# Performance work log

Measured on AMD Instinct MI355X. Metric: run time of the kernel, lower is better.

## Reference

```python
import jax, jax.numpy as jnp
import numpy as np

N_NODES = 50000
N_EDGES = 800000
IN_DIM, HID_DIM, OUT_DIM = 64, 128, 64


def gcn_conv(x, src, dst, W, b, n_nodes):
    # PyG GCNConv default: add self-loops, symmetric normalization D^-1/2 A D^-1/2
    h = x @ W  # [N, F_out]
    ones = jnp.ones(src.shape[0], dtype=x.dtype)
    deg = jax.ops.segment_sum(ones, dst, num_segments=n_nodes)  # in-degree incl. self-loops
    dinv = jnp.where(deg > 0, jax.lax.rsqrt(deg), 0.0).astype(x.dtype)
    norm = dinv[src] * dinv[dst]  # [E]
    msg = h[src] * norm[:, None]  # gather + scale, [E, F_out]
    out = jax.ops.segment_sum(msg, dst, num_segments=n_nodes)  # scatter-add
    return out + b


def setup_inputs() -> dict:
    key = jax.random.key(0)
    k1, k2, k3, k4 = jax.random.split(key, 4)
    z = jax.random.normal(k1, (N_NODES, IN_DIM), dtype=jnp.float32)
    edge_index = jax.random.randint(k2, (2, N_EDGES), 0, N_NODES, dtype=jnp.int64)
    # Glorot-style init for weights, zero bias (PyG defaults)
    W1 = jax.random.normal(k3, (IN_DIM, HID_DIM), dtype=jnp.float32) / np.sqrt(IN_DIM)
    b1 = jnp.zeros((HID_DIM,), dtype=jnp.float32)
    W2 = jax.random.normal(k4, (HID_DIM, OUT_DIM), dtype=jnp.float32) / np.sqrt(HID_DIM)
    b2 = jnp.zeros((OUT_DIM,), dtype=jnp.float32)
    return {"z": z, "edge_index": edge_index, "W1": W1, "b1": b1, "W2": W2, "b2": b2}


def reference(z, edge_index, W1, b1, W2, b2):
    n = z.shape[0]
    loops = jnp.arange(n, dtype=edge_index.dtype)
    src = jnp.concatenate([edge_index[0], loops])
    dst = jnp.concatenate([edge_index[1], loops])
    h = jax.nn.relu(gcn_conv(z, src, dst, W1, b1, n))
    x_hat = gcn_conv(h, src, dst, W2, b2, n)
    return x_hat
```

## Files before the change

### kernel.cpp

```cpp
#include <hip/hip_runtime.h>
#include <hip/hip_bf16.h>

#define N_NODES 50000
#define N_EDGES 800000
#define IN_DIM 64
#define HID_DIM 128
#define OUT_DIM 64
#define NGRP 8
#define NSLC 4
#define NPB 32
#define ECAP 2048
#define NE8 (NGRP * N_NODES)
#define NC8C ((NE8 + 255) / 256)
#define NCMC ((N_NODES + 255) / 256)

__device__ int g_in_f32;
__device__ int g_is64;
__device__ int g_csr[N_EDGES];
__device__ int g_mcsr[N_EDGES];
__device__ int g_deg8[NE8];
__device__ int g_rowptr8[NE8 + 1];
__device__ int g_cursor8[NE8];
__device__ int g_mrp[N_NODES + 1];
__device__ int g_bsum[NC8C];
__device__ int g_bsum2[NCMC];
__device__ float g_dinv[N_NODES];
__device__ __align__(16) float g_W1f[IN_DIM * HID_DIM];
__device__ __align__(16) float g_W2f[HID_DIM * OUT_DIM];
__device__ __align__(16) float g_b1f[HID_DIM];
__device__ __align__(16) float g_b2f[OUT_DIM];
__device__ __align__(16) float g_hs1[(size_t)N_NODES * IN_DIM];
__device__ __align__(16) float g_agg1[(size_t)N_NODES * IN_DIM];

__device__ __forceinline__ float loadx(const void* p, int i, int f32) {
    if (f32) return ((const float*)p)[i];
    unsigned int u = ((unsigned int)((const unsigned short*)p)[i]) << 16;
    return __uint_as_float(u);
}

__global__ __launch_bounds__(256) void zerodet_kernel(const unsigned short* __restrict__ zw,
                                                      const unsigned int* __restrict__ ew,
                                                      int NE, int E) {
    int idx = blockIdx.x * 256 + threadIdx.x;
    if (idx < NE) g_deg8[idx] = 0;
    if (blockIdx.x == 0) {
        __shared__ int flags[2];
        int t = threadIdx.x;
        if (t < 2) flags[t] = 0;
        __syncthreads();
        int hit = 0;
        for (int k = 0; k < 64; k++) {
            int i = 2 * ((t * 64 + k) * 97);
            if (((zw[i] >> 7) & 0xFF) == 0xFF) hit = 1;
        }
        if (hit) atomicOr(&flags[0], 1);
        int nz = 0;
        int step = E / 4096;
        for (int k = 0; k < 4; k++) {
            int i = 1 + 2 * ((t * 4 + k) * step);
            if (ew[i] != 0) nz = 1;
        }
        if (nz) atomicOr(&flags[1], 1);
        __syncthreads();
        if (t == 0) { g_in_f32 = flags[0]; g_is64 = (flags[1] == 0) ? 1 : 0; }
    }
}

__global__ __launch_bounds__(256) void degprep_kernel(const void* __restrict__ ei,
                                                      const void* __restrict__ W1, const void* __restrict__ b1,
                                                      const void* __restrict__ W2, const void* __restrict__ b2,
                                                      int N, int E) {
    int e = blockIdx.x * 256 + threadIdx.x;
    int f32 = g_in_f32;
    if (e < IN_DIM * HID_DIM) g_W1f[e] = loadx(W1, e, f32);
    if (e < HID_DIM * OUT_DIM) g_W2f[e] = loadx(W2, e, f32);
    if (e < HID_DIM) g_b1f[e] = loadx(b1, e, f32);
    if (e < OUT_DIM) g_b2f[e] = loadx(b2, e, f32);
    if (e < E) {
        int d = g_is64 ? (int)((const long long*)ei)[E + e] : ((const int*)ei)[E + e];
        int g = blockIdx.x & (NGRP - 1);
        atomicAdd(&g_deg8[g * N + d], 1);
    }
}

__global__ __launch_bounds__(256) void scans_kernel(int N, int NE) {
    __shared__ int sc[256];
    int t = threadIdx.x;
    int NC8 = (NE + 255) >> 8, NCM = (N + 255) >> 8;
    for (int vb = blockIdx.x; vb < NC8; vb += gridDim.x) {
        int idx = (vb << 8) + t;
        int d = (idx < NE) ? g_deg8[idx] : 0;
        sc[t] = d;
        __syncthreads();
        for (int off = 1; off < 256; off <<= 1) {
            int v = (t >= off) ? sc[t - off] : 0;
            __syncthreads();
            sc[t] += v;
            __syncthreads();
        }
        if (idx < NE) g_rowptr8[idx] = sc[t] - d;
        if (t == 255) g_bsum[vb] = sc[255];
        __syncthreads();
    }
    for (int vb = blockIdx.x; vb < NCM; vb += gridDim.x) {
        int idx = (vb << 8) + t;
        int d = 0;
        if (idx < N) {
#pragma unroll
            for (int g = 0; g < NGRP; g++) d += g_deg8[g * N + idx];
            g_dinv[idx] = rsqrtf((float)d + 1.0f);
        }
        sc[t] = d;
        __syncthreads();
        for (int off = 1; off < 256; off <<= 1) {
            int v = (t >= off) ? sc[t - off] : 0;
            __syncthreads();
            sc[t] += v;
            __syncthreads();
        }
        if (idx < N) g_mrp[idx] = sc[t] - d;
        if (t == 255) g_bsum2[vb] = sc[255];
        __syncthreads();
    }
}

__global__ __launch_bounds__(256) void addoffs_kernel(int N, int NE, int E) {
    __shared__ int sc[256];
    int t = threadIdx.x;
    int vb = blockIdx.x;
    int NCM = (N + 255) >> 8;
    int ps = 0;
    for (int i = t; i < vb; i += 256) ps += g_bsum[i];
    sc[t] = ps;
    __syncthreads();
    for (int off = 128; off > 0; off >>= 1) {
        if (t < off) sc[t] += sc[t + off];
        __syncthreads();
    }
    int prefix = sc[0];
    __syncthreads();
    int idx = vb * 256 + t;
    if (idx < NE) {
        int base = g_rowptr8[idx] + prefix;
        g_rowptr8[idx] = base;
        g_cursor8[idx] = base;
    }
    if (vb < NCM) {
        int ps2 = 0;
        for (int i = t; i < vb; i += 256) ps2 += g_bsum2[i];
        sc[t] = ps2;
        __syncthreads();
        for (int off = 128; off > 0; off >>= 1) {
            if (t < off) sc[t] += sc[t + off];
            __syncthreads();
        }
        int prefix2 = sc[0];
        if (idx < N) g_mrp[idx] += prefix2;
    }
    if (vb == 0 && t == 0) { g_rowptr8[NE] = E; g_mrp[N] = E; }
}

__global__ __launch_bounds__(256) void scatter_kernel(const void* __restrict__ ei, int N, int E) {
    int e = blockIdx.x * 256 + threadIdx.x;
    if (e < E) {
        int s, d;
        if (g_is64) { const long long* p = (const long long*)ei; s = (int)p[e]; d = (int)p[E + e]; }
        else        { const int* p = (const int*)ei; s = p[e]; d = p[E + e]; }
        int g = blockIdx.x & (NGRP - 1);
        int pos = atomicAdd(&g_cursor8[g * N + d], 1);
        g_csr[pos] = s;
    }
}

__global__ __launch_bounds__(256) void mergezp_kernel(const void* __restrict__ z, int N) {
    int gid = blockIdx.x * 256 + threadIdx.x;
    int wid = gid >> 6;
    int lane = threadIdx.x & 63;
    if (wid < N) {
        int mybeg = 0, mycnt = 0;
        if (lane < NGRP) {
            mybeg = g_rowptr8[lane * N + wid];
            mycnt = g_rowptr8[lane * N + wid + 1] - mybeg;
        }
        int incl = mycnt;
#pragma unroll
        for (int off = 1; off < NGRP; off <<= 1) {
            int v = __shfl_up(incl, off, 64);
            if (lane >= off) incl += v;
        }
        int myoff = incl - mycnt;
        int go[NGRP], gb[NGRP];
#pragma unroll
        for (int k = 0; k < NGRP; k++) {
            go[k] = __shfl(myoff, k, 64);
            gb[k] = __shfl(mybeg, k, 64);
        }
        int total = __shfl(incl, NGRP - 1, 64);
        int base = g_mrp[wid];
        for (int i = lane; i < total; i += 64) {
            int g = 0;
#pragma unroll
            for (int k = 1; k < NGRP; k++) g += (i >= go[k]);
            g_mcsr[base + i] = g_csr[gb[g] + i - go[g]];
        }
    }
    if (gid < N * IN_DIM) {
        int node = gid >> 6, c = gid & 63;
        int s = c >> 4, off = c & 15;
        g_agg1[(size_t)s * (N * 16) + node * 16 + off] = loadx(z, gid, g_in_f32) * g_dinv[node];
    }
}

template <int LAYER2>
__global__ __launch_bounds__(256) void aggslc_kernel(void* __restrict__ outp, int N) {
    __shared__ int rp[NPB + 1];
    __shared__ int eidx[ECAP];
    int s = blockIdx.x & (NSLC - 1);
    int n0 = (blockIdx.x >> 2) * NPB;
    int t = threadIdx.x;
    if (t <= NPB) {
        int idx = n0 + t;
        rp[t] = g_mrp[idx <= N ? idx : N];
    }
    __syncthreads();
    int base = rp[0];
    int range = rp[NPB] - base;
    bool staged = (range <= ECAP);
    if (staged) {
        for (int i = t; i < range; i += 256) eidx[i] = g_mcsr[base + i];
    }
    __syncthreads();
    const float* tab = (LAYER2 ? g_hs1 : g_agg1) + (size_t)s * ((size_t)N * 16);
    int lane = t & 63;
    int w8 = (t >> 6) * 8;
    int col = lane & 15, eslot = lane >> 4;
    float res[8];
#pragma unroll
    for (int k = 0; k < 8; k++) {
        int jb = rp[w8 + k] - base + eslot;
        int je = rp[w8 + k + 1] - base;
        float a0 = 0.f, a1 = 0.f, a2 = 0.f, a3 = 0.f;
        int j = jb;
        if (staged) {
            for (; j + 12 < je; j += 16) {
                int i0 = eidx[j], i1 = eidx[j + 4], i2 = eidx[j + 8], i3 = eidx[j + 12];
                a0 += tab[i0 * 16 + col];
                a1 += tab[i1 * 16 + col];
                a2 += tab[i2 * 16 + col];
                a3 += tab[i3 * 16 + col];
            }
            for (; j < je; j += 4) a0 += tab[eidx[j] * 16 + col];
        } else {
            for (; j < je; j += 4) a0 += tab[g_mcsr[base + j] * 16 + col];
        }
        float a = (a0 + a1) + (a2 + a3);
        a += __shfl_xor(a, 16, 64);
        a += __shfl_xor(a, 32, 64);
        res[k] = a;
    }
    if (lane < 16) {
#pragma unroll
        for (int k = 0; k < 8; k++) {
            int nk = n0 + w8 + k;
            if (nk < N) {
                float v = (res[k] + tab[(size_t)nk * 16 + col]) * g_dinv[nk];
                if (LAYER2) {
                    v += g_b2f[s * 16 + col];
                    int oc = nk * 64 + s * 16 + col;
                    if (g_in_f32) ((float*)outp)[oc] = v;
                    else ((__hip_bfloat16*)outp)[oc] = __float2bfloat16(v);
                } else {
                    g_hs1[(size_t)s * ((size_t)N * 16) + nk * 16 + col] = v;
                }
            }
        }
    }
}

__global__ __launch_bounds__(256) void gemm_fused_kernel(int N) {
    __shared__ __align__(16) float B[64 * 132];
    int t = threadIdx.x;
    int row0 = blockIdx.x * 64;
#pragma unroll
    for (int s = 0; s < 4; s++) {
        int i = t + s * 256;
        int r = i >> 4, k4 = i & 15;
        int row = row0 + r;
        int g = k4 >> 2, off = (k4 & 3) * 4;
        float4 v = make_float4(0.f, 0.f, 0.f, 0.f);
        if (row < N) v = *(const float4*)&g_hs1[(size_t)g * (N * 16) + row * 16 + off];
        *(float4*)&B[r * 132 + k4 * 4] = v;
    }
    __syncthreads();
    int cg1 = t & 31, rg1 = t >> 5;
    int c1 = cg1 * 4, r1 = rg1 * 8;
    float acc1[8][4] = {};
#pragma unroll 4
    for (int k = 0; k < IN_DIM; k++) {
        float b[4];
        *(float4*)b = *(const float4*)&g_W1f[k * HID_DIM + c1];
        float a[8];
#pragma unroll
        for (int i = 0; i < 8; i++) a[i] = B[(r1 + i) * 132 + k];
#pragma unroll
        for (int i = 0; i < 8; i++)
#pragma unroll
            for (int j = 0; j < 4; j++) acc1[i][j] = fmaf(a[i], b[j], acc1[i][j]);
    }
    __syncthreads();
    {
        float4 bias = *(const float4*)&g_b1f[c1];
#pragma unroll
        for (int i = 0; i < 8; i++) {
            float4 v;
            v.x = fmaxf(acc1[i][0] + bias.x, 0.f);
            v.y = fmaxf(acc1[i][1] + bias.y, 0.f);
            v.z = fmaxf(acc1[i][2] + bias.z, 0.f);
            v.w = fmaxf(acc1[i][3] + bias.w, 0.f);
            *(float4*)&B[(r1 + i) * 132 + c1] = v;
        }
    }
    __syncthreads();
    {
        int cg = t & 15, rg = t >> 4;
        int c0 = cg * 4, r0 = rg * 4;
        float acc[4][4] = {};
#pragma unroll 2
        for (int k4 = 0; k4 < 32; k4++) {
            float av[4][4];
#pragma unroll
            for (int i = 0; i < 4; i++)
                *(float4*)av[i] = *(const float4*)&B[(r0 + i) * 132 + k4 * 4];
#pragma unroll
            for (int jj = 0; jj < 4; jj++) {
                float b[4];
                *(float4*)b = *(const float4*)&g_W2f[(k4 * 4 + jj) * OUT_DIM + c0];
#pragma unroll
                for (int i = 0; i < 4; i++)
#pragma unroll
                    for (int j = 0; j < 4; j++) acc[i][j] = fmaf(av[i][jj], b[j], acc[i][j]);
            }
        }
        int g = cg >> 2, off = (cg & 3) * 4;
#pragma unroll
        for (int i = 0; i < 4; i++) {
            int row = row0 + r0 + i;
            if (row < N) {
                float dn = g_dinv[row];
                float4 v;
                v.x = acc[i][0] * dn;
                v.y = acc[i][1] * dn;
                v.z = acc[i][2] * dn;
                v.w = acc[i][3] * dn;
                *(float4*)&g_hs1[(size_t)g * (N * 16) + row * 16 + off] = v;
            }
        }
    }
}

extern "C" void kernel_launch(void* const* d_in, const int* in_sizes, int n_in,
                              void* d_out, int out_size, void* d_ws, size_t ws_size,
                              hipStream_t stream) {
    const void* z  = d_in[0];
    const void* ei = d_in[1];
    const void* W1 = d_in[2];
    const void* b1 = d_in[3];
    const void* W2 = d_in[4];
    const void* b2 = d_in[5];

    const int N = in_sizes[0] / IN_DIM;
    const int E = in_sizes[1] / 2;
    const int NE = NGRP * N;
    const int NC8 = (NE + 255) / 256;
    const int aggblocks = NSLC * ((N + NPB - 1) / NPB);

    zerodet_kernel<<<NC8, 256, 0, stream>>>((const unsigned short*)z, (const unsigned int*)ei, NE, E);
    degprep_kernel<<<(E + 255) / 256, 256, 0, stream>>>(ei, W1, b1, W2, b2, N, E);
    scans_kernel<<<NC8, 256, 0, stream>>>(N, NE);
    addoffs_kernel<<<NC8, 256, 0, stream>>>(N, NE, E);
    scatter_kernel<<<(E + 255) / 256, 256, 0, stream>>>(ei, N, E);
    mergezp_kernel<<<(N * 64 + 255) / 256, 256, 0, stream>>>(z, N);

    aggslc_kernel<0><<<aggblocks, 256, 0, stream>>>(d_out, N);
    gemm_fused_kernel<<<(N + 63) / 64, 256, 0, stream>>>(N);
    aggslc_kernel<1><<<aggblocks, 256, 0, stream>>>(d_out, N);
}
```

Measured before the change: 301.3 us.

## Remap aggregation threads to float4 per node and double nodes per block

The gather-aggregate kernel now gives each node to four lanes, each loading a float4 of its 16-column slice. Before, a wavefront walked 8 nodes in turn with scalar loads and reduced across lanes with shuffles. The goal is wider memory transactions, no shuffle reductions, and more nodes in flight per block, with NPB doubled from 32 to 64. In exchange, per-lane load imbalance follows node degree, and the larger node block makes it more likely that a block's edge count exceeds the shared staging capacity, which sends it to the unstaged fallback path.

```diff
diff --git a/kernel.cpp b/kernel.cpp
--- a/kernel.cpp
+++ b/kernel.cpp
@@ -8,7 +8,7 @@
 #define OUT_DIM 64
 #define NGRP 8
 #define NSLC 4
-#define NPB 32
+#define NPB 64
 #define ECAP 2048
 #define NE8 (NGRP * N_NODES)
 #define NC8C ((NE8 + 255) / 256)
@@ -232,48 +232,55 @@
     __syncthreads();
     const float* tab = (LAYER2 ? g_hs1 : g_agg1) + (size_t)s * ((size_t)N * 16);
     int lane = t & 63;
-    int w8 = (t >> 6) * 8;
-    int col = lane & 15, eslot = lane >> 4;
-    float res[8];
-#pragma unroll
-    for (int k = 0; k < 8; k++) {
-        int jb = rp[w8 + k] - base + eslot;
-        int je = rp[w8 + k + 1] - base;
-        float a0 = 0.f, a1 = 0.f, a2 = 0.f, a3 = 0.f;
+    int nsub = (t >> 6) * 16 + (lane >> 2);
+    int col4 = lane & 3;
+    int nk = n0 + nsub;
+    if (nk >= N) return;
+    float4 a0 = make_float4(0.f, 0.f, 0.f, 0.f);
+    float4 a1 = make_float4(0.f, 0.f, 0.f, 0.f);
+    int jb = rp[nsub] - base;
+    int je = rp[nsub + 1] - base;
+    if (staged) {
         int j = jb;
-        if (staged) {
-            for (; j + 12 < je; j += 16) {
-                int i0 = eidx[j], i1 = eidx[j + 4], i2 = eidx[j + 8], i3 = eidx[j + 12];
-                a0 += tab[i0 * 16 + col];
-                a1 += tab[i1 * 16 + col];
-                a2 += tab[i2 * 16 + col];
-                a3 += tab[i3 * 16 + col];
-            }
-            for (; j < je; j += 4) a0 += tab[eidx[j] * 16 + col];
+        for (; j + 1 < je; j += 2) {
+            int i0 = eidx[j], i1 = eidx[j + 1];
+            float4 v0 = *(const float4*)&tab[(size_t)i0 * 16 + col4 * 4];
+            float4 v1 = *(const float4*)&tab[(size_t)i1 * 16 + col4 * 4];
+            a0.x += v0.x; a0.y += v0.y; a0.z += v0.z; a0.w += v0.w;
+            a1.x += v1.x; a1.y += v1.y; a1.z += v1.z; a1.w += v1.w;
+        }
+        if (j < je) {
+            float4 v0 = *(const float4*)&tab[(size_t)eidx[j] * 16 + col4 * 4];
+            a0.x += v0.x; a0.y += v0.y; a0.z += v0.z; a0.w += v0.w;
+        }
+    } else {
+        for (int j = jb; j < je; j++) {
+            float4 v0 = *(const float4*)&tab[(size_t)g_mcsr[base + j] * 16 + col4 * 4];
+            a0.x += v0.x; a0.y += v0.y; a0.z += v0.z; a0.w += v0.w;
+        }
+    }
+    float4 self = *(const float4*)&tab[(size_t)nk * 16 + col4 * 4];
+    float dn = g_dinv[nk];
+    float4 v;
+    v.x = (a0.x + a1.x + self.x) * dn;
+    v.y = (a0.y + a1.y + self.y) * dn;
+    v.z = (a0.z + a1.z + self.z) * dn;
+    v.w = (a0.w + a1.w + self.w) * dn;
+    if (LAYER2) {
+        float4 bias = *(const float4*)&g_b2f[s * 16 + col4 * 4];
+        v.x += bias.x; v.y += bias.y; v.z += bias.z; v.w += bias.w;
+        int oc = nk * 64 + s * 16 + col4 * 4;
+        if (g_in_f32) {
+            *(float4*)&((float*)outp)[oc] = v;
         } else {
-            for (; j < je; j += 4) a0 += tab[g_mcsr[base + j] * 16 + col];
-        }
-        float a = (a0 + a1) + (a2 + a3);
-        a += __shfl_xor(a, 16, 64);
-        a += __shfl_xor(a, 32, 64);
-        res[k] = a;
-    }
-    if (lane < 16) {
-#pragma unroll
-        for (int k = 0; k < 8; k++) {
-            int nk = n0 + w8 + k;
-            if (nk < N) {
-                float v = (res[k] + tab[(size_t)nk * 16 + col]) * g_dinv[nk];
-                if (LAYER2) {
-                    v += g_b2f[s * 16 + col];
-                    int oc = nk * 64 + s * 16 + col;
-                    if (g_in_f32) ((float*)outp)[oc] = v;
-                    else ((__hip_bfloat16*)outp)[oc] = __float2bfloat16(v);
-                } else {
-                    g_hs1[(size_t)s * ((size_t)N * 16) + nk * 16 + col] = v;
-                }
-            }
-        }
+            __hip_bfloat16* o = (__hip_bfloat16*)outp + oc;
+            o[0] = __float2bfloat16(v.x);
+            o[1] = __float2bfloat16(v.y);
+            o[2] = __float2bfloat16(v.z);
+            o[3] = __float2bfloat16(v.w);
+        }
+    } else {
+        *(float4*)&g_hs1[(size_t)s * ((size_t)N * 16) + nk * 16 + col4 * 4] = v;
     }
 }
 
```

Result: faster. 275.2 us (-8.7%).
